# Kernel optimization log

Hardware: AMD Instinct MI355X
Metric: run time of the kernel (lower is better)

Reference implementation:

```python
import jax, jax.numpy as jnp
import numpy as np


def setup_inputs() -> dict:
    key = jax.random.key(0)
    ks = jax.random.split(key, 5)
    B, S, H, I, E = 4, 2048, 1024, 4096, 8
    scale_in = 1.0 / np.sqrt(H)
    scale_mid = 1.0 / np.sqrt(I)
    return {
        "x": jax.random.normal(ks[0], (B, S, H), dtype=jnp.float32),
        "w_gate": jax.random.normal(ks[1], (H, E), dtype=jnp.float32) * scale_in,
        "w1": jax.random.normal(ks[2], (E, H, I), dtype=jnp.float32) * scale_in,
        "w2": jax.random.normal(ks[3], (E, I, H), dtype=jnp.float32) * scale_mid,
        "w3": jax.random.normal(ks[4], (E, H, I), dtype=jnp.float32) * scale_in,
        "num_experts_per_tok": 2,
    }


def reference(x, w_gate, w1, w2, w3, num_experts_per_tok):
    """MoE with top-k routing and SwiGLU experts (Mixtral-style).

    x: [B, S, H]; w_gate: [H, E]; w1/w3: [E, H, I]; w2: [E, I, H].
    Returns [B, S, H]. Matches torch module output (aux_loss is a side
    attribute in the original, not returned).
    """
    B, S, H = x.shape
    E = w_gate.shape[1]
    K = num_experts_per_tok
    xf = x.reshape(-1, H)                           # [T, H]

    logits = xf @ w_gate                            # [T, E]
    probs = jax.nn.softmax(logits, axis=-1)
    topk_probs, topk_idx = jax.lax.top_k(probs, K)  # [T, K]
    topk_probs = topk_probs / topk_probs.sum(axis=-1, keepdims=True)

    # Per-token per-expert combine weight: sum over k of renormalized top-k
    # probs mapped back to expert slots. [T, E]
    comb = jnp.sum(jax.nn.one_hot(topk_idx, E, dtype=xf.dtype)
                   * topk_probs[..., None], axis=1)

    out = jnp.zeros_like(xf)
    for e in range(E):  # small fixed loop over experts
        hidden = jax.nn.silu(xf @ w1[e]) * (xf @ w3[e])  # [T, I]
        out = out + (hidden @ w2[e]) * comb[:, e:e + 1]
    return out.reshape(B, S, H)
```

## Files before the change

### kernel.cpp

```cpp
#include <hip/hip_runtime.h>

typedef unsigned short u16;
typedef __attribute__((ext_vector_type(4))) float f32x4;
typedef __attribute__((ext_vector_type(8))) short s16x8;

#define T_TOK 8192
#define HD    1024
#define ID    4096
#define NE    8
#define AK    (T_TOK * 2)
#define APAD  (AK + 256)
#define MTMAX 72

#define BAR()   __builtin_amdgcn_s_barrier()
#define SB0()   __builtin_amdgcn_sched_barrier(0)
#define PRIO1() __builtin_amdgcn_s_setprio(1)
#define PRIO0() __builtin_amdgcn_s_setprio(0)
#define WAITV6() asm volatile("s_waitcnt vmcnt(6)" ::: "memory")
#define WAITV8() asm volatile("s_waitcnt vmcnt(8)" ::: "memory")
#define LGKM0()  do { asm volatile("s_waitcnt lgkmcnt(0)" ::: "memory"); SB0(); } while (0)

__device__ __forceinline__ u16 f2bf(float f) {
  unsigned u = __builtin_bit_cast(unsigned, f);
  u += 0x7FFFu + ((u >> 16) & 1u);
  return (u16)(u >> 16);
}

__device__ __forceinline__ float bf2f(u16 v) {
  unsigned u = (unsigned)v << 16;
  return __builtin_bit_cast(float, u);
}

__device__ __forceinline__ void gld16(u16* lds, const u16* g) {
  __builtin_amdgcn_global_load_lds(
      (const __attribute__((address_space(1))) unsigned int*)g,
      (__attribute__((address_space(3))) unsigned int*)lds, 16, 0, 0);
}

__device__ __forceinline__ int decode_tile(const int* __restrict__ counts,
                                           int ti, int& e, int& m0,
                                           int& aoff, int& cnt) {
  int s = 0;
  for (int ee = 0; ee < NE; ++ee) {
    int c = counts[ee];
    int nt = (c + 255) >> 8;
    if (ti < nt) { e = ee; m0 = ti << 8; aoff = s; cnt = c; return 1; }
    ti -= nt; s += c;
  }
  return 0;
}


__global__ __launch_bounds__(256) void k_scatter(
    const int* __restrict__ tidx, const int* __restrict__ counts,
    int* cursors, int* __restrict__ list, int* __restrict__ pos) {
  int idx = blockIdx.x * 256 + threadIdx.x;
  if (idx >= AK) return;
  int e = tidx[idx];
  int off = 0;
  for (int ee = 0; ee < NE; ++ee) off += (ee < e) ? counts[ee] : 0;
  int p = atomicAdd(&cursors[e], 1);
  int a = off + p;
  list[a] = idx >> 1;
  pos[idx] = a;
}


#define NBP_T13 4096
#define NBP_RTR 2048

__global__ __launch_bounds__(256) void k_prep(
    const float* __restrict__ x, const float* __restrict__ wg,
    const float* __restrict__ w1, const float* __restrict__ w3,
    u16* __restrict__ xb, u16* __restrict__ w13b,
    int* __restrict__ tidx, float* __restrict__ tw, int* __restrict__ counts) {
  __shared__ char smem[256 * 72 * 2];
  int bid = blockIdx.x, t = threadIdx.x;

  if (bid < NBP_T13) {
    u16 (*tile)[72] = (u16(*)[72])smem;
    int bx = bid & 63;
    int by = (bid >> 6) & 3;
    int bz = bid >> 8;
    int which = bz >> 3, e = bz & 7;
    const float* in = (which ? w3 : w1) + (size_t)e * HD * ID;
    int r0 = by * 256, c0 = bx * 64;
    int rr = t >> 4, cc4 = (t & 15) * 4;
#pragma unroll
    for (int i = 0; i < 16; ++i) {
      int r = i * 16 + rr;
      float4 v = *(const float4*)&in[(size_t)(r0 + r) * ID + c0 + cc4];
      ushort4 bv;
      bv.x = f2bf(v.x); bv.y = f2bf(v.y); bv.z = f2bf(v.z); bv.w = f2bf(v.w);
      *(ushort4*)&tile[r][cc4] = bv;
    }
    __syncthreads();
    int w = t >> 6, c = t & 63;
    int gc = c0 + c;
    int orow = ((gc >> 4) << 5) + which * 16 + (gc & 15);
    u16* obase = w13b + ((size_t)e * 2 * ID + orow) * HD + r0 + w * 64;
#pragma unroll
    for (int j = 0; j < 8; ++j) {
      s16x8 o;
#pragma unroll
      for (int q = 0; q < 8; ++q) o[q] = (short)tile[w * 64 + j * 8 + q][c];
      *(s16x8*)&obase[j * 8] = o;
    }
    return;
  }
  {
    float* wgs = (float*)smem;
    int blockR = bid - NBP_T13;
    for (int i = t; i < NE * HD; i += 256) {
      int h = i >> 3, e = i & 7;
      wgs[e * HD + h] = wg[i];
    }
    __syncthreads();
    int lane = t & 63, wid = t >> 6;
    int tok = blockR * 4 + wid;
    const float* xr = x + (size_t)tok * HD;
    u16* xo = xb + (size_t)tok * HD;
    double acc[NE];
#pragma unroll
    for (int e = 0; e < NE; ++e) acc[e] = 0.0;
    for (int i = 0; i < HD / 64; ++i) {
      float xv = xr[lane + i * 64];
      xo[lane + i * 64] = f2bf(xv);
#pragma unroll
      for (int e = 0; e < NE; ++e)
        acc[e] += (double)xv * (double)wgs[e * HD + lane + i * 64];
    }
#pragma unroll
    for (int e = 0; e < NE; ++e)
      for (int s = 32; s >= 1; s >>= 1) acc[e] += __shfl_xor(acc[e], s, 64);
    int e0 = 0; double m0 = acc[0];
    for (int e = 1; e < NE; ++e) if (acc[e] > m0) { m0 = acc[e]; e0 = e; }
    int e1 = -1; double m1 = -1e300;
    for (int e = 0; e < NE; ++e) if (e != e0 && acc[e] > m1) { m1 = acc[e]; e1 = e; }
    if (lane == 0) {
      double d = exp(m1 - m0);
      tidx[tok * 2] = e0; tidx[tok * 2 + 1] = e1;
      tw[tok * 2] = (float)(1.0 / (1.0 + d));
      tw[tok * 2 + 1] = (float)(d / (1.0 + d));
      atomicAdd(&counts[e0], 1);
      atomicAdd(&counts[e1], 1);
    }
  }
}


#define GEMM_CORE(NTK, NITER) \
  int wr = wid >> 2, wc = wid & 3; \
  int lane15 = lane & 15, lq = lane >> 4, sw8 = lane15 & 7; \
  f32x4 acc[8][4]; \
  _Pragma("unroll") for (int m = 0; m < 8; ++m) \
    _Pragma("unroll") for (int n = 0; n < 4; ++n) acc[m][n] = (f32x4){0.f,0.f,0.f,0.f}; \
  auto stgA = [&](int bb, int h, int kt) { \
    gld16(&As[bb][(h*128 + 0*64 + wid*8) * 64], gA[h*2+0] + kt*64); \
    gld16(&As[bb][(h*128 + 1*64 + wid*8) * 64], gA[h*2+1] + kt*64); }; \
  auto stgB = [&](int bb, int h, int kt) { \
    gld16(&Bs[bb][(h*128 + 0*64 + wid*8) * 64], gB[h*2+0] + kt*64); \
    gld16(&Bs[bb][(h*128 + 1*64 + wid*8) * 64], gB[h*2+1] + kt*64); }; \
  s16x8 a[4][2], b[4][2]; \
  auto rdA = [&](int bb, int mh) { \
    _Pragma("unroll") for (int mm = 0; mm < 4; ++mm) \
      _Pragma("unroll") for (int kk = 0; kk < 2; ++kk) \
        a[mm][kk] = *(const s16x8*)&As[bb][(mh*128 + wr*64 + mm*16 + lane15)*64 + (((kk*4+lq)^sw8)*8)]; }; \
  auto rdB = [&](int bb, int fh) { \
    _Pragma("unroll") for (int ff = 0; ff < 2; ++ff) \
      _Pragma("unroll") for (int kk = 0; kk < 2; ++kk) \
        b[fh*2+ff][kk] = *(const s16x8*)&Bs[bb][(fh*128 + wc*32 + ff*16 + lane15)*64 + (((kk*4+lq)^sw8)*8)]; }; \
  auto mf = [&](int mh, int fh) { \
    _Pragma("unroll") for (int kk = 0; kk < 2; ++kk) \
      _Pragma("unroll") for (int mm = 0; mm < 4; ++mm) \
        _Pragma("unroll") for (int ff = 0; ff < 2; ++ff) \
          acc[mh*4+mm][fh*2+ff] = __builtin_amdgcn_mfma_f32_16x16x32_bf16(a[mm][kk], b[fh*2+ff][kk], acc[mh*4+mm][fh*2+ff], 0, 0, 0); }; \
   \
  stgA(0,0,0); stgB(0,0,0); stgA(0,1,0); stgB(0,1,0); stgA(1,0,1); stgB(1,0,1); \
  WAITV8(); BAR(); SB0(); \
  for (int i = 0; i < (NITER); ++i) { \
    int ku2 = (2*i+2) & ((NTK)-1), ku3 = (2*i+3) & ((NTK)-1); \
     rdA(0,0); rdB(0,0); stgA(1,1,2*i+1); WAITV6(); BAR(); LGKM0(); PRIO1(); mf(0,0); PRIO0(); BAR(); SB0(); \
     rdB(0,1); stgB(1,1,2*i+1); BAR(); LGKM0(); PRIO1(); mf(0,1); PRIO0(); BAR(); SB0(); \
     rdA(0,1); stgA(0,0,ku2); BAR(); LGKM0(); PRIO1(); mf(1,0); PRIO0(); BAR(); SB0(); \
     stgB(0,0,ku2); WAITV8(); BAR(); PRIO1(); mf(1,1); PRIO0(); BAR(); SB0(); \
     rdA(1,0); rdB(1,0); stgA(0,1,ku2); WAITV6(); BAR(); LGKM0(); PRIO1(); mf(0,0); PRIO0(); BAR(); SB0(); \
     rdB(1,1); stgB(0,1,ku2); BAR(); LGKM0(); PRIO1(); mf(0,1); PRIO0(); BAR(); SB0(); \
     rdA(1,1); stgA(1,0,ku3); BAR(); LGKM0(); PRIO1(); mf(1,0); PRIO0(); BAR(); SB0(); \
     stgB(1,0,ku3); WAITV8(); BAR(); PRIO1(); mf(1,1); PRIO0(); BAR(); SB0(); \
  }

#define NGEMM1 (32 * MTMAX)
#define NGEMM2 (16 * MTMAX)

__global__ __launch_bounds__(512, 1) void k_gemm1(
    const u16* __restrict__ xb, const u16* __restrict__ w13b,
    const int* __restrict__ list, const int* __restrict__ counts,
    u16* __restrict__ hidden,
    const float* __restrict__ w2, u16* __restrict__ w2b) {
  __shared__ u16 As[2][256 * 64];
  __shared__ u16 Bs[2][256 * 64];
  int tid = threadIdx.x, lane = tid & 63, wid = tid >> 6;
  int bid = blockIdx.x;

  if (bid >= NGEMM1) {
    u16 (*tile)[64] = (u16(*)[64])&As[0][0];
    int flat = bid - NGEMM1;
    int bx = flat & 15, by = (flat >> 4) & 15, e2 = flat >> 8;
    const float* in = w2 + (size_t)e2 * ID * HD;
    u16* outp = w2b + (size_t)e2 * HD * ID;
    int r0 = by * 256, c0 = bx * 64;
    int rr = tid >> 4, cc4 = (tid & 15) * 4;
#pragma unroll
    for (int i = 0; i < 8; ++i) {
      int r = i * 32 + rr;
      float4 v = *(const float4*)&in[(size_t)(r0 + r) * HD + c0 + cc4];
      ushort4 bv;
      bv.x = f2bf(v.x); bv.y = f2bf(v.y); bv.z = f2bf(v.z); bv.w = f2bf(v.w);
      *(ushort4*)&tile[r][cc4] = bv;
    }
    __syncthreads();
    int w = tid >> 6, c = tid & 63;
    u16* obase = outp + (size_t)(c0 + c) * ID + r0 + w * 32;
#pragma unroll
    for (int j = 0; j < 4; ++j) {
      s16x8 o;
#pragma unroll
      for (int q = 0; q < 8; ++q) o[q] = (short)tile[w * 32 + j * 8 + q][c];
      *(s16x8*)&obase[j * 8] = o;
    }
    return;
  }

  int work = (bid & 7) * (NGEMM1 / 8) + (bid >> 3);
  int nx = work / MTMAX;
  int ti = work % MTMAX;
  int e, m0, aoff, cnt;
  if (!decode_tile(counts, ti, e, m0, aoff, cnt)) return;
  int n0 = nx * 256;

  int l8 = lane >> 3, c8 = lane & 7;
  int csrc = (c8 ^ l8) * 8;

  const u16* gA[4]; const u16* gB[4];
#pragma unroll
  for (int h = 0; h < 2; ++h)
#pragma unroll
    for (int c = 0; c < 2; ++c) {
      int row = h * 128 + c * 64 + wid * 8 + l8;
      int rr = m0 + row; if (rr > cnt - 1) rr = cnt - 1;
      gA[h*2+c] = xb + (size_t)list[aoff + rr] * HD + csrc;
      gB[h*2+c] = w13b + ((size_t)e * 2 * ID + n0 + row) * HD + csrc;
    }

  GEMM_CORE(HD / 64, HD / 128)

  u16 (*Ls)[132] = (u16(*)[132])&As[0][0];
  BAR();
#pragma unroll
  for (int mh = 0; mh < 2; ++mh)
#pragma unroll
    for (int mm = 0; mm < 4; ++mm)
#pragma unroll
      for (int j = 0; j < 4; ++j) {
        int rl = mh * 128 + wr * 64 + mm * 16 + lq * 4 + j;
#pragma unroll
        for (int p = 0; p < 2; ++p) {
          float v1 = acc[mh*4+mm][2*p][j];
          float v3 = acc[mh*4+mm][2*p+1][j];
          float s = v1 / (1.0f + __expf(-v1));
          Ls[rl][p * 64 + wc * 16 + lane15] = f2bf(s * v3);
        }
      }
  BAR();
#pragma unroll
  for (int ps = 0; ps < 8; ++ps) {
    int r = ps * 32 + (tid >> 4);
    int grow = m0 + r;
    if (grow < cnt) {
      int cl = (tid & 15) * 8;
      *(s16x8*)&hidden[(size_t)(aoff + grow) * ID + (n0 >> 1) + cl] =
          *(const s16x8*)&Ls[r][cl];
    }
  }
}

__global__ __launch_bounds__(512, 1) void k_gemm2(
    const u16* __restrict__ hidden, const u16* __restrict__ w2b,
    const int* __restrict__ counts,
    u16* __restrict__ yp0, u16* __restrict__ yp3) {
  int bid = blockIdx.x;
  int work = (bid & 7) * (NGEMM2 / 8) + (bid >> 3);
  int px = work / MTMAX;
  int ti = work % MTMAX;
  int e, m0, aoff, cnt;
  if (!decode_tile(counts, ti, e, m0, aoff, cnt)) return;
  int n0 = (px & 3) * 256;
  int kidx = px >> 2;
  int kc = kidx * 1024;

  __shared__ u16 As[2][256 * 64];
  __shared__ u16 Bs[2][256 * 64];

  int tid = threadIdx.x, lane = tid & 63, wid = tid >> 6;
  int l8 = lane >> 3, c8 = lane & 7;
  int csrc = (c8 ^ l8) * 8;

  const u16* gA[4]; const u16* gB[4];
#pragma unroll
  for (int h = 0; h < 2; ++h)
#pragma unroll
    for (int c = 0; c < 2; ++c) {
      int row = h * 128 + c * 64 + wid * 8 + l8;
      gA[h*2+c] = hidden + (size_t)(aoff + m0 + row) * ID + kc + csrc;
      gB[h*2+c] = w2b + ((size_t)e * HD + n0 + row) * ID + kc + csrc;
    }

  GEMM_CORE(1024 / 64, 1024 / 128)

  u16* yp = (kidx < 3) ? yp0 + (size_t)kidx * AK * HD : yp3;
  u16 (*Ls)[132] = (u16(*)[132])&As[0][0];
#pragma unroll
  for (int half = 0; half < 2; ++half) {
    BAR();
#pragma unroll
    for (int mh = 0; mh < 2; ++mh)
#pragma unroll
      for (int mm = 0; mm < 4; ++mm)
#pragma unroll
        for (int j = 0; j < 4; ++j) {
          int rl = mh * 128 + wr * 64 + mm * 16 + lq * 4 + j;
#pragma unroll
          for (int fo = 0; fo < 2; ++fo) {
            int f = half * 2 + fo;
            Ls[rl][wc * 32 + fo * 16 + lane15] = f2bf(acc[mh*4+mm][f][j]);
          }
        }
    BAR();
#pragma unroll
    for (int ps = 0; ps < 8; ++ps) {
      int r = ps * 32 + (tid >> 4);
      int grow = m0 + r;
      if (grow < cnt) {
        int cl = (tid & 15) * 8;
        *(s16x8*)&yp[(size_t)(aoff + grow) * HD + n0 + half * 128 + cl] =
            *(const s16x8*)&Ls[r][cl];
      }
    }
  }
}

__global__ __launch_bounds__(256) void k_combine(
    const u16* __restrict__ yp0, const u16* __restrict__ yp3,
    const int* __restrict__ pos, const float* __restrict__ tw,
    float* __restrict__ out) {
  int t = blockIdx.x;
  int c = threadIdx.x * 4;
  int a0 = pos[t * 2], a1 = pos[t * 2 + 1];
  float w0 = tw[t * 2], w1 = tw[t * 2 + 1];
  float s0[4] = {0.f, 0.f, 0.f, 0.f}, s1[4] = {0.f, 0.f, 0.f, 0.f};
#pragma unroll
  for (int k = 0; k < 4; ++k) {
    const u16* yp = (k < 3) ? yp0 + (size_t)k * AK * HD : yp3;
    ushort4 v0 = *(const ushort4*)&yp[(size_t)a0 * HD + c];
    ushort4 v1 = *(const ushort4*)&yp[(size_t)a1 * HD + c];
    s0[0] += bf2f(v0.x); s0[1] += bf2f(v0.y); s0[2] += bf2f(v0.z); s0[3] += bf2f(v0.w);
    s1[0] += bf2f(v1.x); s1[1] += bf2f(v1.y); s1[2] += bf2f(v1.z); s1[3] += bf2f(v1.w);
  }
  float4 o;
  o.x = w0 * s0[0] + w1 * s1[0];
  o.y = w0 * s0[1] + w1 * s1[1];
  o.z = w0 * s0[2] + w1 * s1[2];
  o.w = w0 * s0[3] + w1 * s1[3];
  *(float4*)&out[(size_t)t * HD + c] = o;
}


extern "C" void kernel_launch(void* const* d_in, const int* in_sizes, int n_in,
                              void* d_out, int out_size, void* d_ws, size_t ws_size,
                              hipStream_t stream) {
  const float* x  = (const float*)d_in[0];
  const float* wg = (const float*)d_in[1];
  const float* w1 = (const float*)d_in[2];
  const float* w2 = (const float*)d_in[3];
  const float* w3 = (const float*)d_in[4];

  char* p = (char*)d_ws;
  auto alloc = [&](size_t bytes) {
    char* r = p;
    p += (bytes + 255) & ~(size_t)255;
    return r;
  };
  u16*   xb      = (u16*)alloc((size_t)T_TOK * HD * 2);
  u16*   w13b    = (u16*)alloc((size_t)NE * 2 * ID * HD * 2);
  u16*   w2b     = (u16*)alloc((size_t)NE * HD * ID * 2);
  u16*   hidden  = (u16*)alloc((size_t)APAD * ID * 2);
  u16*   yp3     = (u16*)alloc((size_t)AK * HD * 2);
  int*   tidx    = (int*)alloc(AK * 4);
  float* tw      = (float*)alloc(AK * 4);
  int*   list    = (int*)alloc(AK * 4);
  int*   pos     = (int*)alloc(AK * 4);
  int*   counts  = (int*)alloc(64);
  int*   cursors = counts + 8;
  (void)ws_size; (void)in_sizes; (void)n_in; (void)out_size;

  u16* yp0 = w13b;

  hipMemsetAsync(counts, 0, 64, stream);
  k_prep<<<NBP_T13 + NBP_RTR, 256, 0, stream>>>(
      x, wg, w1, w3, xb, w13b, tidx, tw, counts);
  k_scatter<<<AK / 256, 256, 0, stream>>>(tidx, counts, cursors, list, pos);

  k_gemm1<<<NGEMM1 + 2048, 512, 0, stream>>>(xb, w13b, list, counts, hidden,
                                             w2, w2b);
  k_gemm2<<<NGEMM2, 512, 0, stream>>>(hidden, w2b, counts, yp0, yp3);
  k_combine<<<T_TOK, 256, 0, stream>>>(yp0, yp3, pos, tw, (float*)d_out);
}
```

Before: 861.8 us.

## Reshape weight-transpose tiles and switch GEMM grids to 2D block mapping

The w1/w3 bf16 transpose in k_prep now uses 128x128 tiles instead of 256x64, so each output row segment covers more contiguous columns. The GEMM kernels drop the XCD-aware remapping of a flat block id (bid&7 striding) and index tiles directly through a 2D grid (blockIdx.x for N/K chunks, blockIdx.y for the token tile). The aim is simpler indexing and a different traversal order that may change L2 reuse of weights versus activations. The risk is losing the per-XCD locality that the old swizzle provided.

```diff
diff --git a/kernel.cpp b/kernel.cpp
--- a/kernel.cpp
+++ b/kernel.cpp
@@ -74,36 +74,36 @@
     const float* __restrict__ w1, const float* __restrict__ w3,
     u16* __restrict__ xb, u16* __restrict__ w13b,
     int* __restrict__ tidx, float* __restrict__ tw, int* __restrict__ counts) {
-  __shared__ char smem[256 * 72 * 2];
+  __shared__ char smem[128 * 136 * 2];
   int bid = blockIdx.x, t = threadIdx.x;
 
   if (bid < NBP_T13) {
-    u16 (*tile)[72] = (u16(*)[72])smem;
-    int bx = bid & 63;
-    int by = (bid >> 6) & 3;
+    u16 (*tile)[136] = (u16(*)[136])smem;
+    int bx = bid & 31;
+    int by = (bid >> 5) & 7;
     int bz = bid >> 8;
     int which = bz >> 3, e = bz & 7;
     const float* in = (which ? w3 : w1) + (size_t)e * HD * ID;
-    int r0 = by * 256, c0 = bx * 64;
-    int rr = t >> 4, cc4 = (t & 15) * 4;
+    int r0 = by * 128, c0 = bx * 128;
+    int rr = t >> 5, cc4 = (t & 31) * 4;
 #pragma unroll
     for (int i = 0; i < 16; ++i) {
-      int r = i * 16 + rr;
+      int r = i * 8 + rr;
       float4 v = *(const float4*)&in[(size_t)(r0 + r) * ID + c0 + cc4];
       ushort4 bv;
       bv.x = f2bf(v.x); bv.y = f2bf(v.y); bv.z = f2bf(v.z); bv.w = f2bf(v.w);
       *(ushort4*)&tile[r][cc4] = bv;
     }
     __syncthreads();
-    int w = t >> 6, c = t & 63;
+    int half = t >> 7, c = t & 127;
     int gc = c0 + c;
     int orow = ((gc >> 4) << 5) + which * 16 + (gc & 15);
-    u16* obase = w13b + ((size_t)e * 2 * ID + orow) * HD + r0 + w * 64;
+    u16* obase = w13b + ((size_t)e * 2 * ID + orow) * HD + r0 + half * 64;
 #pragma unroll
     for (int j = 0; j < 8; ++j) {
       s16x8 o;
 #pragma unroll
-      for (int q = 0; q < 8; ++q) o[q] = (short)tile[w * 64 + j * 8 + q][c];
+      for (int q = 0; q < 8; ++q) o[q] = (short)tile[half * 64 + j * 8 + q][c];
       *(s16x8*)&obase[j * 8] = o;
     }
     return;
@@ -190,9 +190,6 @@
      stgB(1,0,ku3); WAITV8(); BAR(); PRIO1(); mf(1,1); PRIO0(); BAR(); SB0(); \
   }
 
-#define NGEMM1 (32 * MTMAX)
-#define NGEMM2 (16 * MTMAX)
-
 __global__ __launch_bounds__(512, 1) void k_gemm1(
     const u16* __restrict__ xb, const u16* __restrict__ w13b,
     const int* __restrict__ list, const int* __restrict__ counts,
@@ -201,11 +198,10 @@
   __shared__ u16 As[2][256 * 64];
   __shared__ u16 Bs[2][256 * 64];
   int tid = threadIdx.x, lane = tid & 63, wid = tid >> 6;
-  int bid = blockIdx.x;
-
-  if (bid >= NGEMM1) {
+
+  if (blockIdx.y >= MTMAX) {
     u16 (*tile)[64] = (u16(*)[64])&As[0][0];
-    int flat = bid - NGEMM1;
+    int flat = (blockIdx.y - MTMAX) * 32 + blockIdx.x;
     int bx = flat & 15, by = (flat >> 4) & 15, e2 = flat >> 8;
     const float* in = w2 + (size_t)e2 * ID * HD;
     u16* outp = w2b + (size_t)e2 * HD * ID;
@@ -232,12 +228,9 @@
     return;
   }
 
-  int work = (bid & 7) * (NGEMM1 / 8) + (bid >> 3);
-  int nx = work / MTMAX;
-  int ti = work % MTMAX;
   int e, m0, aoff, cnt;
-  if (!decode_tile(counts, ti, e, m0, aoff, cnt)) return;
-  int n0 = nx * 256;
+  if (!decode_tile(counts, blockIdx.y, e, m0, aoff, cnt)) return;
+  int n0 = blockIdx.x * 256;
 
   int l8 = lane >> 3, c8 = lane & 7;
   int csrc = (c8 ^ l8) * 8;
@@ -289,14 +282,10 @@
     const u16* __restrict__ hidden, const u16* __restrict__ w2b,
     const int* __restrict__ counts,
     u16* __restrict__ yp0, u16* __restrict__ yp3) {
-  int bid = blockIdx.x;
-  int work = (bid & 7) * (NGEMM2 / 8) + (bid >> 3);
-  int px = work / MTMAX;
-  int ti = work % MTMAX;
   int e, m0, aoff, cnt;
-  if (!decode_tile(counts, ti, e, m0, aoff, cnt)) return;
-  int n0 = (px & 3) * 256;
-  int kidx = px >> 2;
+  if (!decode_tile(counts, blockIdx.y, e, m0, aoff, cnt)) return;
+  int n0 = (blockIdx.x & 3) * 256;
+  int kidx = blockIdx.x >> 2;
   int kc = kidx * 1024;
 
   __shared__ u16 As[2][256 * 64];
@@ -411,8 +400,9 @@
       x, wg, w1, w3, xb, w13b, tidx, tw, counts);
   k_scatter<<<AK / 256, 256, 0, stream>>>(tidx, counts, cursors, list, pos);
 
-  k_gemm1<<<NGEMM1 + 2048, 512, 0, stream>>>(xb, w13b, list, counts, hidden,
-                                             w2, w2b);
-  k_gemm2<<<NGEMM2, 512, 0, stream>>>(hidden, w2b, counts, yp0, yp3);
+  dim3 gg1(2 * ID / 256, MTMAX + 64, 1);
+  k_gemm1<<<gg1, 512, 0, stream>>>(xb, w13b, list, counts, hidden, w2, w2b);
+  dim3 gg2(16, MTMAX, 1);
+  k_gemm2<<<gg2, 512, 0, stream>>>(hidden, w2b, counts, yp0, yp3);
   k_combine<<<T_TOK, 256, 0, stream>>>(yp0, yp3, pos, tw, (float*)d_out);
 }
```

Result: no change. 867.0 us (+0.6%).
